# Optimization experiments

Hardware: AMD Instinct MI355X
Metric: run time of the kernel (lower is better)

The kernel has to match this reference:

```python
import jax, jax.numpy as jnp
import numpy as np
import math

D_MODEL = 2048
N_HEADS = 16
HEAD_DIM = D_MODEL // N_HEADS  # 128
SEQ = 2048
BATCH = 1


def make_freqs(seq_len, head_dim, theta=10000.0):
    # standard rotary frequencies: freqs_cis = exp(i * t * inv_freq)
    inv_freq = 1.0 / (theta ** (np.arange(0, head_dim, 2, dtype=np.float32) / head_dim))
    t = np.arange(seq_len, dtype=np.float32)
    ang = np.outer(t, inv_freq)  # [seq, head_dim/2]
    return jnp.asarray(np.cos(ang)), jnp.asarray(np.sin(ang))


def setup_inputs() -> dict:
    key = jax.random.key(0)
    ks = jax.random.split(key, 6)
    x = jax.random.normal(ks[0], (BATCH, SEQ, D_MODEL), dtype=jnp.float32)
    freqs_cos, freqs_sin = make_freqs(SEQ, HEAD_DIM)
    # causal additive mask, broadcastable to [b, h, s, s]
    mask = jnp.where(jnp.tril(jnp.ones((SEQ, SEQ), dtype=bool)), 0.0, -1e9).astype(jnp.float32)[None, None]
    scale = 0.02
    wq = jax.random.normal(ks[1], (D_MODEL, D_MODEL), dtype=jnp.float32) * scale
    wk = jax.random.normal(ks[2], (D_MODEL, D_MODEL), dtype=jnp.float32) * scale
    wv = jax.random.normal(ks[3], (D_MODEL, D_MODEL), dtype=jnp.float32) * scale
    wo = jax.random.normal(ks[4], (D_MODEL, D_MODEL), dtype=jnp.float32) * scale
    return {"x": x, "freqs_cos": freqs_cos, "freqs_sin": freqs_sin, "mask": mask,
            "wq": wq, "wk": wk, "wv": wv, "wo": wo}


def _apply_rotary(q, k, cos, sin):
    # q, k: [b, s, h, hd]; cos/sin: [s, hd/2]
    def rot(t):
        tr = t.reshape(*t.shape[:-1], -1, 2)  # [b, s, h, hd/2, 2]
        re, im = tr[..., 0], tr[..., 1]
        c = cos[None, :, None, :]
        s = sin[None, :, None, :]
        # complex multiply (re + i im) * (c + i s)
        out_re = re * c - im * s
        out_im = re * s + im * c
        return jnp.stack([out_re, out_im], axis=-1).reshape(t.shape)
    return rot(q), rot(k)


def reference(x, freqs_cos, freqs_sin, mask, wq, wk, wv, wo):
    b, s, _ = x.shape
    # QKV projections (nn.Linear with no bias: x @ W^T; W is square so use x @ W
    # with W stored already-transposed -- weights here are random so x @ W is faithful math)
    q = (x @ wq).reshape(b, s, N_HEADS, HEAD_DIM)
    k = (x @ wk).reshape(b, s, N_HEADS, HEAD_DIM)
    v = (x @ wv).reshape(b, s, N_HEADS, HEAD_DIM)
    q, k = _apply_rotary(q, k, freqs_cos, freqs_sin)
    # [b, h, s_q, s_k]
    scores = jnp.einsum("bqhd,bkhd->bhqk", q, k) / math.sqrt(HEAD_DIM)
    scores = scores + mask
    probs = jax.nn.softmax(scores.astype(jnp.float32), axis=-1).astype(q.dtype)
    out = jnp.einsum("bhqk,bkhd->bqhd", probs, v).reshape(b, s, N_HEADS * HEAD_DIM)
    return out @ wo
```

## Files before the change

kernel.cpp:

```cpp
#include <hip/hip_runtime.h>
#include <hip/hip_bf16.h>
#include <math.h>

#define SEQ 2048
#define DM 2048
#define NH 16
#define HD 128
#define QKV_N 6144

typedef __bf16 bf16;
typedef __bf16 bf16x8 __attribute__((ext_vector_type(8)));
typedef __bf16 bf16x4v __attribute__((ext_vector_type(4)));
typedef __bf16 bf16x2v __attribute__((ext_vector_type(2)));
typedef float f32x4 __attribute__((ext_vector_type(4)));

__device__ inline int sw_idx32(int row, int quad) {
    return (row * 4 + (quad ^ ((row >> 1) & 3))) * 8;
}
__device__ inline int sw_idx64(int row, int chunk) {
    return (row * 8 + (chunk ^ (row & 7))) * 8;
}

__device__ inline void async16(const void* g, void* l) {
    __builtin_amdgcn_global_load_lds((const __attribute__((address_space(1))) void*)g,
                                     (__attribute__((address_space(3))) void*)l, 16, 0, 0);
}

__global__ void k_prep(const float* __restrict__ wq, const float* __restrict__ wk,
                       const float* __restrict__ wv, const float* __restrict__ wo,
                       bf16* __restrict__ wT, bf16* __restrict__ woT,
                       const float* __restrict__ x, bf16* __restrict__ xb,
                       const float* __restrict__ fc, const float* __restrict__ fs,
                       bf16* __restrict__ csT) {
    const int z = blockIdx.z;
    int tx = threadIdx.x, ty = threadIdx.y;
    if (z == 4) {
        int bid = blockIdx.y * 64 + blockIdx.x;
        if (bid >= 1024) return;
        int i = bid * 1024 + ty * 32 + tx;
        float4 v = ((const float4*)x)[i];
        bf16x4v o;
        o.x = (bf16)v.x; o.y = (bf16)v.y; o.z = (bf16)v.z; o.w = (bf16)v.w;
        ((bf16x4v*)xb)[i] = o;
        return;
    }
    if (z == 5) {
        int bid = blockIdx.y * 64 + blockIdx.x;
        if (bid >= 128) return;
        int idx = bid * 1024 + ty * 32 + tx;
        bf16x2v cs;
        cs.x = (bf16)fc[idx];
        cs.y = (bf16)fs[idx];
        ((bf16x2v*)csT)[idx] = cs;
        return;
    }
    __shared__ float tile[32][33];
    const float* src = (z == 0) ? wq : (z == 1) ? wk : (z == 2) ? wv : wo;
    bf16* dst = (z < 3) ? (wT + (size_t)z * DM * DM) : woT;
    int bx = blockIdx.x * 32, by = blockIdx.y * 32;
    tile[ty][tx] = src[(size_t)(by + ty) * DM + bx + tx];
    __syncthreads();
    int n = bx + ty;
    if (z < 2) {
        int nh = n & 127;
        n = (n & ~127) | (((nh >> 5) << 5) + ((nh & 1) << 4) + ((nh & 31) >> 1));
    }
    dst[(size_t)n * DM + by + tx] = (bf16)tile[tx][ty];
}

__global__ __launch_bounds__(256) void k_gemm_qkv(const bf16* __restrict__ A,
                                                  const bf16* __restrict__ Bt,
                                                  bf16* __restrict__ qkv,
                                                  bf16* __restrict__ vT,
                                                  const bf16* __restrict__ csT) {
    const int K = DM;
    __shared__ bf16 smem[2 * 128 * 64];
    bf16* As = smem;
    bf16* Bs = smem + 128 * 64;
    const int t = threadIdx.x;
    const int lane = t & 63;
    const int w = t >> 6;
    const int wr = (w >> 1) * 64, wc = (w & 1) * 64;
    const int l15 = lane & 15, quad = lane >> 4;
    const size_t bm = (size_t)blockIdx.y * 128, bn = (size_t)blockIdx.x * 128;
    f32x4 acc[4][4];
#pragma unroll
    for (int i = 0; i < 4; ++i)
#pragma unroll
        for (int j = 0; j < 4; ++j) acc[i][j] = (f32x4){0.f, 0.f, 0.f, 0.f};

    int srow[4], sgc[4];
#pragma unroll
    for (int j = 0; j < 4; ++j) {
        int c = j * 256 + t;
        srow[j] = c >> 3;
        sgc[j] = ((c & 7) ^ (srow[j] & 7)) * 8;
    }

    for (int kt = 0; kt < K; kt += 64) {
#pragma unroll
        for (int j = 0; j < 4; ++j) {
            async16(&A[(bm + srow[j]) * K + kt + sgc[j]], &As[(j * 256 + t) * 8]);
            async16(&Bt[(bn + srow[j]) * K + kt + sgc[j]], &Bs[(j * 256 + t) * 8]);
        }
        __syncthreads();
#pragma unroll
        for (int kh = 0; kh < 2; ++kh) {
            bf16x8 af[4], bfm[4];
#pragma unroll
            for (int mi = 0; mi < 4; ++mi)
                af[mi] = *(const bf16x8*)&As[sw_idx64(wr + mi * 16 + l15, kh * 4 + quad)];
#pragma unroll
            for (int ni = 0; ni < 4; ++ni)
                bfm[ni] = *(const bf16x8*)&Bs[sw_idx64(wc + ni * 16 + l15, kh * 4 + quad)];
#pragma unroll
            for (int mi = 0; mi < 4; ++mi)
#pragma unroll
                for (int ni = 0; ni < 4; ++ni)
                    acc[mi][ni] = __builtin_amdgcn_mfma_f32_16x16x32_bf16(
                        af[mi], bfm[ni], acc[mi][ni], 0, 0, 0);
        }
        __syncthreads();
    }

    if (blockIdx.x < 32) {
#pragma unroll
        for (int j = 0; j < 8; ++j) {
            int c = j * 256 + t;
            int row = c >> 4;
            int g16 = ((c & 15) ^ (row & 15)) * 8;
            async16(&csT[(bm + row) * 128 + g16], &smem[c * 8]);
        }
        __syncthreads();
        const bf16x2v* cs32 = (const bf16x2v*)smem;
#pragma unroll
        for (int mi = 0; mi < 4; ++mi)
#pragma unroll
            for (int r = 0; r < 4; ++r) {
                const int row_l = wr + mi * 16 + quad * 4 + r;
                const int rk = row_l & 15;
#pragma unroll
                for (int g = 0; g < 2; ++g) {
                    const int base_i = ((wc + 32 * g) & 127) >> 1;
                    const int word_i = base_i + l15;
                    const int slot = (word_i >> 2) ^ rk;
                    bf16x2v cs = cs32[(row_l * 16 + slot) * 4 + (word_i & 3)];
                    float c = (float)cs.x, sn = (float)cs.y;
                    float re = acc[mi][2 * g][r];
                    float im = acc[mi][2 * g + 1][r];
                    bf16x2v o;
                    o.x = (bf16)(re * c - im * sn);
                    o.y = (bf16)(re * sn + im * c);
                    *(bf16x2v*)&qkv[(bm + row_l) * QKV_N + bn + wc + 32 * g + 2 * l15] = o;
                }
            }
    } else {
#pragma unroll
        for (int mi = 0; mi < 4; ++mi)
#pragma unroll
            for (int ni = 0; ni < 4; ++ni) {
                const int n_local = wc + ni * 16 + l15;
#pragma unroll
                for (int r = 0; r < 4; ++r) {
                    int s_local = wr + mi * 16 + quad * 4 + r;
                    smem[n_local * 128 + ((((s_local >> 3) ^ (n_local & 15)) * 8) |
                                          (s_local & 7))] = (bf16)acc[mi][ni][r];
                }
            }
        __syncthreads();
        const int n_l = t >> 1;
        const size_t ch = bn - 4096 + n_l;
#pragma unroll
        for (int j = 0; j < 8; ++j) {
            int c = (t & 1) * 8 + j;
            bf16x8 v = *(const bf16x8*)&smem[n_l * 128 + ((c ^ (n_l & 15)) * 8)];
            *(bf16x8*)&vT[ch * SEQ + bm + c * 8] = v;
        }
    }
}

template <typename OutT, int BN>
__global__ __launch_bounds__(256) void k_gemm_bt(const bf16* __restrict__ A,
                                                 const bf16* __restrict__ Bt,
                                                 OutT* __restrict__ C,
                                                 int M, int N, int K) {
    constexpr int NI = BN / 32;
    __shared__ bf16 As[128 * 64];
    __shared__ bf16 Bs[BN * 64];
    const int t = threadIdx.x;
    const int lane = t & 63;
    const int w = t >> 6;
    const int wr = (w >> 1) * 64, wc = (w & 1) * (BN / 2);
    const int l15 = lane & 15, quad = lane >> 4;
    const size_t bm = (size_t)blockIdx.y * 128, bn = (size_t)blockIdx.x * BN;
    f32x4 acc[4][NI];
#pragma unroll
    for (int i = 0; i < 4; ++i)
#pragma unroll
        for (int j = 0; j < NI; ++j) acc[i][j] = (f32x4){0.f, 0.f, 0.f, 0.f};

    for (int kt = 0; kt < K; kt += 64) {
#pragma unroll
        for (int j = 0; j < 4; ++j) {
            int c = j * 256 + t;
            int row = c >> 3, g = ((c & 7) ^ (row & 7)) * 8;
            async16(&A[(bm + row) * K + kt + g], &As[c * 8]);
        }
#pragma unroll
        for (int j = 0; j < NI; ++j) {
            int c = j * 256 + t;
            int row = c >> 3, g = ((c & 7) ^ (row & 7)) * 8;
            async16(&Bt[(bn + row) * K + kt + g], &Bs[c * 8]);
        }
        __syncthreads();
#pragma unroll
        for (int kh = 0; kh < 2; ++kh) {
            bf16x8 af[4], bfm[NI];
#pragma unroll
            for (int mi = 0; mi < 4; ++mi)
                af[mi] = *(const bf16x8*)&As[sw_idx64(wr + mi * 16 + l15, kh * 4 + quad)];
#pragma unroll
            for (int ni = 0; ni < NI; ++ni)
                bfm[ni] = *(const bf16x8*)&Bs[sw_idx64(wc + ni * 16 + l15, kh * 4 + quad)];
#pragma unroll
            for (int mi = 0; mi < 4; ++mi)
#pragma unroll
                for (int ni = 0; ni < NI; ++ni)
                    acc[mi][ni] = __builtin_amdgcn_mfma_f32_16x16x32_bf16(
                        af[mi], bfm[ni], acc[mi][ni], 0, 0, 0);
        }
        __syncthreads();
    }
#pragma unroll
    for (int mi = 0; mi < 4; ++mi)
#pragma unroll
        for (int ni = 0; ni < NI; ++ni)
#pragma unroll
            for (int r = 0; r < 4; ++r) {
                size_t row = bm + wr + mi * 16 + quad * 4 + r;
                size_t col = bn + wc + ni * 16 + l15;
                C[row * (size_t)N + col] = (OutT)acc[mi][ni][r];
            }
}

__global__ __launch_bounds__(256) void k_flash(const bf16* __restrict__ qkv,
                                               const bf16* __restrict__ vT,
                                               bf16* __restrict__ out) {
    __shared__ bf16 Ks[4][64 * 32];
    __shared__ bf16 Vs[2][128 * 32];
    __shared__ bf16 Pl[4][16][72];
    const int t = threadIdx.x;
    const int lane = t & 63;
    const int w = t >> 6;
    const int l15 = lane & 15, quad = lane >> 4;
    const int b = blockIdx.x;
    const int h = (b & 7) * 2 + ((b >> 3) & 1);
    const int qb = 31 - (b >> 4);
    const int q0w = qb * 64 + w * 16;
    const float sc = 0.08838834764831845f;

    const size_t qrow = (size_t)(q0w + l15) * QKV_N + h * HD;
    bf16x8 aq[4];
#pragma unroll
    for (int u = 0; u < 4; ++u)
        aq[u] = *(const bf16x8*)&qkv[qrow + u * 32 + quad * 8];

    f32x4 o[8];
#pragma unroll
    for (int c = 0; c < 8; ++c) o[c] = (f32x4){0.f, 0.f, 0.f, 0.f};
    float l_r[4] = {0.f, 0.f, 0.f, 0.f};

    const int srow = t >> 2;
    const int ch = ((t & 3) ^ ((t >> 3) & 3)) * 8;

    for (int kt = 0; kt <= qb; ++kt) {
        const int kbase = kt * 64;
#pragma unroll
        for (int u = 0; u < 4; ++u)
            async16(&qkv[(size_t)(kbase + srow) * QKV_N + DM + h * HD + u * 32 + ch],
                    &Ks[u][t * 8]);
#pragma unroll
        for (int j = 0; j < 2; ++j) {
            async16(&vT[(size_t)(h * HD + srow) * SEQ + kbase + j * 32 + ch],
                    &Vs[j][t * 8]);
            async16(&vT[(size_t)(h * HD + 64 + srow) * SEQ + kbase + j * 32 + ch],
                    &Vs[j][(t + 256) * 8]);
        }
        __syncthreads();
        f32x4 s[4];
#pragma unroll
        for (int sub = 0; sub < 4; ++sub) {
            f32x4 z = (f32x4){0.f, 0.f, 0.f, 0.f};
#pragma unroll
            for (int u = 0; u < 4; ++u) {
                bf16x8 kb = *(const bf16x8*)&Ks[u][sw_idx32(sub * 16 + l15, quad)];
                z = __builtin_amdgcn_mfma_f32_16x16x32_bf16(aq[u], kb, z, 0, 0, 0);
            }
            s[sub] = z;
        }
        const bool masked = (kt == qb);
#pragma unroll
        for (int sub = 0; sub < 4; ++sub)
#pragma unroll
            for (int r = 0; r < 4; ++r) {
                float p = __expf(s[sub][r] * sc);
                if (masked)
                    p = (kbase + sub * 16 + l15 <= q0w + quad * 4 + r) ? p : 0.f;
                l_r[r] += p;
                Pl[w][quad * 4 + r][sub * 16 + l15] = (bf16)p;
            }
        __syncthreads();
        bf16x8 pf0 = *(const bf16x8*)&Pl[w][l15][quad * 8];
        bf16x8 pf1 = *(const bf16x8*)&Pl[w][l15][32 + quad * 8];
#pragma unroll
        for (int c = 0; c < 8; ++c) {
            bf16x8 vb0 = *(const bf16x8*)&Vs[0][sw_idx32(c * 16 + l15, quad)];
            o[c] = __builtin_amdgcn_mfma_f32_16x16x32_bf16(pf0, vb0, o[c], 0, 0, 0);
            bf16x8 vb1 = *(const bf16x8*)&Vs[1][sw_idx32(c * 16 + l15, quad)];
            o[c] = __builtin_amdgcn_mfma_f32_16x16x32_bf16(pf1, vb1, o[c], 0, 0, 0);
        }
        __syncthreads();
    }

    float rl[4];
#pragma unroll
    for (int r = 0; r < 4; ++r) {
        float l = l_r[r];
        l += __shfl_xor(l, 1, 16);
        l += __shfl_xor(l, 2, 16);
        l += __shfl_xor(l, 4, 16);
        l += __shfl_xor(l, 8, 16);
        rl[r] = 1.0f / l;
    }
#pragma unroll
    for (int c = 0; c < 8; ++c)
#pragma unroll
        for (int r = 0; r < 4; ++r)
            out[(size_t)(q0w + quad * 4 + r) * DM + h * HD + c * 16 + l15] =
                (bf16)(o[c][r] * rl[r]);
}

extern "C" void kernel_launch(void* const* d_in, const int* in_sizes, int n_in,
                              void* d_out, int out_size, void* d_ws, size_t ws_size,
                              hipStream_t stream) {
    const float* x  = (const float*)d_in[0];
    const float* fc = (const float*)d_in[1];
    const float* fs = (const float*)d_in[2];
    const float* wq = (const float*)d_in[4];
    const float* wk = (const float*)d_in[5];
    const float* wv = (const float*)d_in[6];
    const float* wo = (const float*)d_in[7];
    float* out = (float*)d_out;

    char* ws = (char*)d_ws;
    bf16* xb  = (bf16*)(ws);
    bf16* wT  = (bf16*)(ws + (size_t)(8u  << 20));
    bf16* woT = (bf16*)(ws + (size_t)(32u << 20));
    bf16* qkv = (bf16*)(ws + (size_t)(40u << 20));
    bf16* vT  = (bf16*)(ws + (size_t)(64u << 20));
    bf16* csT = (bf16*)(ws + (size_t)(72u << 20));

    k_prep<<<dim3(64, 64, 6), dim3(32, 32), 0, stream>>>(wq, wk, wv, wo, wT, woT,
                                                         x, xb, fc, fs, csT);
    k_gemm_qkv<<<dim3(48, 16), 256, 0, stream>>>(xb, wT, qkv, vT, csT);
    k_flash<<<512, 256, 0, stream>>>(qkv, vT, xb);
    k_gemm_bt<float, 64><<<dim3(32, 16), 256, 0, stream>>>(xb, woT, out, SEQ, DM, DM);
}
```

Measured before the change: 327.5 us.

## Move rotary embedding out of QKV GEMM epilogue into separate kernel

Removes the Wq/Wk column permutation and the fused rotary epilogue from the QKV GEMM, which now writes raw Q/K values with scalar bf16 stores. A new k_rope kernel applies the rotation in place over Q and K using 8-wide vector loads. Separately, the flash kernel's block barrier between writing and reading the per-wave P tile is replaced by an LDS waitcnt, since each wave only touches its own slice. This adds a kernel launch and an extra pass over Q/K memory, and the GEMM epilogue stores become narrow, uncoalesced 2-byte writes.

New measurement: 332.7 us. No clear change (+1.6%).

```diff
diff --git a/kernel.cpp b/kernel.cpp
--- a/kernel.cpp
+++ b/kernel.cpp
@@ -60,19 +60,32 @@
     int bx = blockIdx.x * 32, by = blockIdx.y * 32;
     tile[ty][tx] = src[(size_t)(by + ty) * DM + bx + tx];
     __syncthreads();
-    int n = bx + ty;
-    if (z < 2) {
-        int nh = n & 127;
-        n = (n & ~127) | (((nh >> 5) << 5) + ((nh & 1) << 4) + ((nh & 31) >> 1));
-    }
-    dst[(size_t)n * DM + by + tx] = (bf16)tile[tx][ty];
+    dst[(size_t)(bx + ty) * DM + by + tx] = (bf16)tile[tx][ty];
+}
+
+__global__ __launch_bounds__(256) void k_rope(bf16* __restrict__ qkv,
+                                              const bf16* __restrict__ csT) {
+    int idx = blockIdx.x * 256 + threadIdx.x;
+    int s = idx >> 9;
+    int col = (idx & 511) * 8;
+    int dh = col & 127;
+    bf16x8 v = *(const bf16x8*)&qkv[(size_t)s * QKV_N + col];
+    bf16x8 cs = *(const bf16x8*)&csT[s * 128 + dh];
+    bf16x8 o;
+#pragma unroll
+    for (int j = 0; j < 4; ++j) {
+        float re = (float)v[2 * j], im = (float)v[2 * j + 1];
+        float c = (float)cs[2 * j], sn = (float)cs[2 * j + 1];
+        o[2 * j]     = (bf16)(re * c - im * sn);
+        o[2 * j + 1] = (bf16)(re * sn + im * c);
+    }
+    *(bf16x8*)&qkv[(size_t)s * QKV_N + col] = o;
 }
 
 __global__ __launch_bounds__(256) void k_gemm_qkv(const bf16* __restrict__ A,
                                                   const bf16* __restrict__ Bt,
                                                   bf16* __restrict__ qkv,
-                                                  bf16* __restrict__ vT,
-                                                  const bf16* __restrict__ csT) {
+                                                  bf16* __restrict__ vT) {
     const int K = DM;
     __shared__ bf16 smem[2 * 128 * 64];
     bf16* As = smem;
@@ -125,35 +138,14 @@
 
     if (blockIdx.x < 32) {
 #pragma unroll
-        for (int j = 0; j < 8; ++j) {
-            int c = j * 256 + t;
-            int row = c >> 4;
-            int g16 = ((c & 15) ^ (row & 15)) * 8;
-            async16(&csT[(bm + row) * 128 + g16], &smem[c * 8]);
-        }
-        __syncthreads();
-        const bf16x2v* cs32 = (const bf16x2v*)smem;
-#pragma unroll
         for (int mi = 0; mi < 4; ++mi)
 #pragma unroll
-            for (int r = 0; r < 4; ++r) {
-                const int row_l = wr + mi * 16 + quad * 4 + r;
-                const int rk = row_l & 15;
-#pragma unroll
-                for (int g = 0; g < 2; ++g) {
-                    const int base_i = ((wc + 32 * g) & 127) >> 1;
-                    const int word_i = base_i + l15;
-                    const int slot = (word_i >> 2) ^ rk;
-                    bf16x2v cs = cs32[(row_l * 16 + slot) * 4 + (word_i & 3)];
-                    float c = (float)cs.x, sn = (float)cs.y;
-                    float re = acc[mi][2 * g][r];
-                    float im = acc[mi][2 * g + 1][r];
-                    bf16x2v o;
-                    o.x = (bf16)(re * c - im * sn);
-                    o.y = (bf16)(re * sn + im * c);
-                    *(bf16x2v*)&qkv[(bm + row_l) * QKV_N + bn + wc + 32 * g + 2 * l15] = o;
+            for (int ni = 0; ni < 4; ++ni)
+#pragma unroll
+                for (int r = 0; r < 4; ++r) {
+                    size_t row = bm + wr + mi * 16 + quad * 4 + r;
+                    qkv[row * QKV_N + bn + wc + ni * 16 + l15] = (bf16)acc[mi][ni][r];
                 }
-            }
     } else {
 #pragma unroll
         for (int mi = 0; mi < 4; ++mi)
@@ -309,7 +301,7 @@
                 l_r[r] += p;
                 Pl[w][quad * 4 + r][sub * 16 + l15] = (bf16)p;
             }
-        __syncthreads();
+        __asm__ __volatile__("s_waitcnt lgkmcnt(0)" ::: "memory");
         bf16x8 pf0 = *(const bf16x8*)&Pl[w][l15][quad * 8];
         bf16x8 pf1 = *(const bf16x8*)&Pl[w][l15][32 + quad * 8];
 #pragma unroll
@@ -362,7 +354,8 @@
 
     k_prep<<<dim3(64, 64, 6), dim3(32, 32), 0, stream>>>(wq, wk, wv, wo, wT, woT,
                                                          x, xb, fc, fs, csT);
-    k_gemm_qkv<<<dim3(48, 16), 256, 0, stream>>>(xb, wT, qkv, vT, csT);
+    k_gemm_qkv<<<dim3(48, 16), 256, 0, stream>>>(xb, wT, qkv, vT);
+    k_rope<<<4096, 256, 0, stream>>>(qkv, csT);
     k_flash<<<512, 256, 0, stream>>>(qkv, vT, xb);
     k_gemm_bt<float, 64><<<dim3(32, 16), 256, 0, stream>>>(xb, woT, out, SEQ, DM, DM);
 }
```
